# Optimization experiments

Hardware: AMD Instinct MI355X
Metric: run time of the kernel (lower is better)

Reference implementation:

```python
import jax, jax.numpy as jnp
import numpy as np

B, T, C, H = 8, 1024, 1024, 16  # batch, seq, n_embd, n_head


def setup_inputs() -> dict:
    key = jax.random.key(0)
    ks = jax.random.split(key, 5)
    scale = 1.0 / np.sqrt(C)
    return {
        "x": jax.random.normal(ks[0], (B, T, C), dtype=jnp.float32),
        "Wqkv": jax.random.normal(ks[1], (C, 3 * C), dtype=jnp.float32) * scale,
        "bqkv": jax.random.normal(ks[2], (3 * C,), dtype=jnp.float32) * 0.02,
        "Wproj": jax.random.normal(ks[3], (C, C), dtype=jnp.float32) * scale,
        "bproj": jax.random.normal(ks[4], (C,), dtype=jnp.float32) * 0.02,
        "n_head": H,
    }


def reference(x, Wqkv, bqkv, Wproj, bproj, n_head):
    Bb, Tt, Cc = x.shape
    hd = Cc // n_head  # head dim
    qkv = x @ Wqkv + bqkv                      # [B,T,3C]
    q, k, v = jnp.split(qkv, 3, axis=-1)       # each [B,T,C]
    # [B,T,C] -> [B,H,T,hd]
    def to_heads(t):
        return t.reshape(Bb, Tt, n_head, hd).transpose(0, 2, 1, 3)
    q, k, v = to_heads(q), to_heads(k), to_heads(v)
    scores = jnp.einsum("bhqd,bhkd->bhqk", q, k) / jnp.sqrt(jnp.asarray(hd, q.dtype))
    causal = jnp.tril(jnp.ones((Tt, Tt), dtype=bool))
    scores = jnp.where(causal, scores, jnp.asarray(-jnp.inf, scores.dtype))
    attn = jax.nn.softmax(scores, axis=-1)
    y = jnp.einsum("bhqk,bhkd->bhqd", attn, v)  # [B,H,T,hd]
    y = y.transpose(0, 2, 1, 3).reshape(Bb, Tt, Cc)
    return y @ Wproj + bproj
```

## Files before the change

### kernel.cpp

```cpp
#include <hip/hip_runtime.h>
#include <hip/hip_bf16.h>
#include <math.h>
#include <type_traits>

#define Bz 8
#define Tz 1024
#define Cz 1024
#define Hz 16
#define HDz 64
#define Mz (Bz*Tz)
#define N1 (3*Cz)

typedef __attribute__((ext_vector_type(8))) short short8;
typedef __attribute__((ext_vector_type(4))) short short4v;
typedef __attribute__((ext_vector_type(4))) float floatx4;

__device__ __forceinline__ unsigned short f2bf(float f) {
    unsigned u = __float_as_uint(f);
    return (unsigned short)((u + 0x7FFFu + ((u >> 16) & 1u)) >> 16);
}

__device__ __forceinline__ unsigned pkbf(float a, float b) {
    __hip_bfloat162 h = __float22bfloat162_rn(make_float2(a, b));
    return *(unsigned*)&h;
}

__device__ __forceinline__ void gload16(const void* g, void* l) {
    __builtin_amdgcn_global_load_lds(
        (const __attribute__((address_space(1))) unsigned int*)g,
        (__attribute__((address_space(3))) unsigned int*)l, 16, 0, 0);
}

__global__ __launch_bounds__(256) void prep_kernel(
    const float* __restrict__ x, unsigned short* __restrict__ xb,
    const float* __restrict__ Wqkv, unsigned short* __restrict__ Wqkvt,
    const float* __restrict__ Wproj, unsigned short* __restrict__ Wprojt)
{
    __shared__ float tile[32][33];
    const int bid = blockIdx.x;
    const int tid = threadIdx.x;
    if (bid < 8192) {
        int i = bid * 256 + tid;
        float4 v = *(const float4*)&x[(size_t)i * 4];
        ushort4 o;
        o.x = f2bf(v.x); o.y = f2bf(v.y); o.z = f2bf(v.z); o.w = f2bf(v.w);
        *(ushort4*)&xb[(size_t)i * 4] = o;
        return;
    }
    const float* W; unsigned short* Wt; int K, N, n0, k0;
    if (bid < 11264) {
        int b = bid - 8192;  W = Wqkv;  Wt = Wqkvt;  K = Cz; N = N1;
        n0 = (b % 96) * 32;  k0 = (b / 96) * 32;
    } else {
        int b = bid - 11264; W = Wproj; Wt = Wprojt; K = Cz; N = Cz;
        n0 = (b % 32) * 32;  k0 = (b / 32) * 32;
    }
    const int tx = tid & 31, ty = tid >> 5;
#pragma unroll
    for (int i = 0; i < 4; ++i)
        tile[ty + i * 8][tx] = W[(size_t)(k0 + ty + i * 8) * N + n0 + tx];
    __syncthreads();
#pragma unroll
    for (int i = 0; i < 4; ++i)
        Wt[(size_t)(n0 + ty + i * 8) * K + k0 + tx] = f2bf(tile[tx][ty + i * 8]);
}

__global__ __launch_bounds__(256) void vtrans_kernel(const unsigned short* __restrict__ qkvb,
    unsigned short* __restrict__ Vt)
{
    __shared__ unsigned short tile[64][72];
    const int t0 = blockIdx.x * 64;
    const int bh = blockIdx.y;
    const int b = bh >> 4, h = bh & 15;
    const int tid = threadIdx.x;
#pragma unroll
    for (int it = 0; it < 2; ++it) {
        int idx = tid + it * 256;
        int tl = idx >> 3, d8 = idx & 7;
        *(short8*)&tile[tl][d8 * 8] =
            *(const short8*)&qkvb[(size_t)(b * Tz + t0 + tl) * N1 + 2 * Cz + h * HDz + d8 * 8];
    }
    __syncthreads();
#pragma unroll
    for (int it = 0; it < 2; ++it) {
        int idx = tid + it * 256;
        int d = idx >> 3, t8 = idx & 7;
        unsigned short o[8];
#pragma unroll
        for (int j = 0; j < 8; ++j) o[j] = tile[t8 * 8 + j][d];
        *(short8*)&Vt[(size_t)bh * (HDz * Tz) + (size_t)d * Tz + t0 + t8 * 8] = *(short8*)o;
    }
}

__global__ __launch_bounds__(256) void gemm_kernel(const unsigned short* __restrict__ A,
    const unsigned short* __restrict__ Bt, const float* __restrict__ bias,
    void* __restrict__ Cout, int M, int N, int K, int outBf16)
{
    __shared__ unsigned short As[128 * 64];
    __shared__ unsigned short Bs[128 * 64];
    const int tid = threadIdx.x;
    const int lane = tid & 63;
    const int w = tid >> 6, wr = w >> 1, wc = w & 1;
    const int quad = lane >> 4, m16 = lane & 15;
    const int row0 = blockIdx.y * 128, col0 = blockIdx.x * 128;

    float bv[4];
#pragma unroll
    for (int ni = 0; ni < 4; ++ni)
        bv[ni] = bias[col0 + wc * 64 + ni * 16 + m16];

    floatx4 acc[4][4];
#pragma unroll
    for (int mi = 0; mi < 4; ++mi)
#pragma unroll
        for (int ni = 0; ni < 4; ++ni)
            acc[mi][ni] = (floatx4){0.f, 0.f, 0.f, 0.f};

    const int l3 = lane >> 3;
    const int swz = ((lane & 7) ^ l3) * 8;
    const unsigned short* gA[4];
    const unsigned short* gB[4];
    unsigned short* lA[4];
    unsigned short* lB[4];
#pragma unroll
    for (int i = 0; i < 4; ++i) {
        int c = w * 4 + i;
        gA[i] = A  + (size_t)(row0 + c * 8 + l3) * K + swz;
        gB[i] = Bt + (size_t)(col0 + c * 8 + l3) * K + swz;
        lA[i] = &As[c * 512];
        lB[i] = &Bs[c * 512];
    }
    const int sw7 = m16 & 7;

    for (int k0 = 0; k0 < K; k0 += 64) {
#pragma unroll
        for (int i = 0; i < 4; ++i) {
            gload16(gA[i] + k0, lA[i]);
            gload16(gB[i] + k0, lB[i]);
        }
        __syncthreads();
#pragma unroll
        for (int s = 0; s < 2; ++s) {
            short8 af[4], bfr[4];
            const int ch = ((s * 4 + quad) ^ sw7) * 8;
#pragma unroll
            for (int mi = 0; mi < 4; ++mi)
                af[mi] = *(short8*)&As[(wr * 64 + mi * 16 + m16) * 64 + ch];
#pragma unroll
            for (int ni = 0; ni < 4; ++ni)
                bfr[ni] = *(short8*)&Bs[(wc * 64 + ni * 16 + m16) * 64 + ch];
#pragma unroll
            for (int mi = 0; mi < 4; ++mi)
#pragma unroll
                for (int ni = 0; ni < 4; ++ni)
                    acc[mi][ni] = __builtin_amdgcn_mfma_f32_16x16x32_bf16(af[mi], bfr[ni], acc[mi][ni], 0, 0, 0);
        }
        __syncthreads();
    }

#pragma unroll
    for (int mi = 0; mi < 4; ++mi)
#pragma unroll
        for (int ni = 0; ni < 4; ++ni)
#pragma unroll
            for (int reg = 0; reg < 4; ++reg) {
                int r = row0 + wr * 64 + mi * 16 + quad * 4 + reg;
                int c = col0 + wc * 64 + ni * 16 + m16;
                float v = acc[mi][ni][reg] + bv[ni];
                if (outBf16) ((unsigned short*)Cout)[(size_t)r * N + c] = f2bf(v);
                else         ((float*)Cout)[(size_t)r * N + c] = v;
            }
}

__global__ __launch_bounds__(128) void attn_kernel(const unsigned short* __restrict__ qkvb,
    const unsigned short* __restrict__ VtG, unsigned short* __restrict__ attb)
{
    __shared__ unsigned short Ks[2][64 * 64];
    __shared__ unsigned short Vs[2][64 * 64];

    const int bx = blockIdx.x;
    const int bh = blockIdx.y;
    const int b = bh >> 4, h = bh & 15;
    const int tid = threadIdx.x, lane = tid & 63, w = tid >> 6;
    const int quad = lane >> 4, m16 = lane & 15;
    const int qis[2] = {15 - bx, bx};

    const unsigned short* Kb = qkvb + (size_t)(b * Tz) * N1 + Cz + h * HDz;
    const unsigned short* Vb = VtG + (size_t)bh * (HDz * Tz);

    const int l3 = lane >> 3, l7 = lane & 7;
    const int gsw = ((l7 ^ l3) << 3);
    const int sw = m16 & 7;
    const int p0 = (quad ^ sw) << 3;

    short8 onesf = (short8){0,0,0,0,0,0,0,0};
    if (m16 == 0) {
        const short one = (short)0x3F80;
        onesf = (short8){one,one,one,one,one,one,one,one};
    }

    int srow[4];
#pragma unroll
    for (int i = 0; i < 4; ++i) srow[i] = w * 32 + i * 8 + l3;

#pragma unroll
    for (int i = 0; i < 4; ++i) {
        gload16(Kb + (size_t)srow[i] * N1 + gsw, &Ks[0][(w * 4 + i) * 512]);
        gload16(Vb + (size_t)srow[i] * Tz + gsw, &Vs[0][(w * 4 + i) * 512]);
    }

    int buf = 0;
    for (int t = 0; t < 2; ++t) {
        const int qi = qis[t];

        short8 qf[2][2];
        int qrow[2];
#pragma unroll
        for (int mi = 0; mi < 2; ++mi) {
            qrow[mi] = qi * 64 + w * 32 + mi * 16 + m16;
            const size_t rq = (size_t)(b * Tz + qrow[mi]) * N1 + h * HDz;
            qf[mi][0] = *(const short8*)&qkvb[rq + quad * 8];
            qf[mi][1] = *(const short8*)&qkvb[rq + 32 + quad * 8];
        }

        floatx4 of[2][4];
#pragma unroll
        for (int mi = 0; mi < 2; ++mi)
#pragma unroll
            for (int dc = 0; dc < 4; ++dc) of[mi][dc] = (floatx4){0.f, 0.f, 0.f, 0.f};
        floatx4 lsum[2];
        lsum[0] = (floatx4){0.f, 0.f, 0.f, 0.f};
        lsum[1] = (floatx4){0.f, 0.f, 0.f, 0.f};

        auto tile_body = [&](auto diag_c) {
            constexpr bool DIAG = decltype(diag_c)::value;
            constexpr int M0MAX = 4;
            short8 pf[2][2];
#pragma unroll
            for (int m0 = 0; m0 < M0MAX; ++m0) {
                if (DIAG && w == 0 && m0 >= 2) continue;
                const unsigned short* kr = &Ks[buf][(m0 * 16 + m16) * 64];
                short8 kf0 = *(const short8*)&kr[p0];
                short8 kf1 = *(const short8*)&kr[p0 ^ 32];
#pragma unroll
                for (int mi = 0; mi < 2; ++mi) {
                    floatx4 st = (floatx4){0.f, 0.f, 0.f, 0.f};
                    st = __builtin_amdgcn_mfma_f32_16x16x32_bf16(kf0, qf[mi][0], st, 0, 0, 0);
                    st = __builtin_amdgcn_mfma_f32_16x16x32_bf16(kf1, qf[mi][1], st, 0, 0, 0);
                    float p[4];
#pragma unroll
                    for (int reg = 0; reg < 4; ++reg) {
                        p[reg] = exp2f(st[reg] * 0.18033688f);
                        if (DIAG) {
                            int key = m0 * 16 + quad * 4 + reg;
                            int qr  = w * 32 + mi * 16 + m16;
                            p[reg] = (key <= qr) ? p[reg] : 0.f;
                        }
                    }
                    unsigned* pp = (unsigned*)&pf[mi][m0 >> 1];
                    pp[(m0 & 1) * 2 + 0] = pkbf(p[0], p[1]);
                    pp[(m0 & 1) * 2 + 1] = pkbf(p[2], p[3]);
                }
            }
#pragma unroll
            for (int kg = 0; kg < 2; ++kg) {
                if (DIAG && w == 0 && kg == 1) continue;
#pragma unroll
                for (int mi = 0; mi < 2; ++mi)
                    lsum[mi] = __builtin_amdgcn_mfma_f32_16x16x32_bf16(onesf, pf[mi][kg], lsum[mi], 0, 0, 0);
#pragma unroll
                for (int dc = 0; dc < 4; ++dc) {
                    const unsigned short* vrow = &Vs[buf][(dc * 16 + m16) * 64];
                    const int g0 = kg * 4 + (quad >> 1);
                    const int off = (quad & 1) * 4;
                    short4v v0 = *(const short4v*)&vrow[((g0 ^ sw) << 3) + off];
                    short4v v1 = *(const short4v*)&vrow[(((g0 + 2) ^ sw) << 3) + off];
                    short8 vf;
                    vf[0] = v0[0]; vf[1] = v0[1]; vf[2] = v0[2]; vf[3] = v0[3];
                    vf[4] = v1[0]; vf[5] = v1[1]; vf[6] = v1[2]; vf[7] = v1[3];
#pragma unroll
                    for (int mi = 0; mi < 2; ++mi)
                        of[mi][dc] = __builtin_amdgcn_mfma_f32_16x16x32_bf16(vf, pf[mi][kg], of[mi][dc], 0, 0, 0);
                }
            }
        };

        for (int ki = 0; ki <= qi; ++ki) {
            __syncthreads();
            const int nk = (ki < qi) ? (ki + 1) : (t == 0 ? 0 : -1);
            if (nk >= 0) {
                const size_t ko = (size_t)nk * 64;
#pragma unroll
                for (int i = 0; i < 4; ++i) {
                    gload16(Kb + (ko + srow[i]) * N1 + gsw, &Ks[buf ^ 1][(w * 4 + i) * 512]);
                    gload16(Vb + (size_t)srow[i] * Tz + ko + gsw, &Vs[buf ^ 1][(w * 4 + i) * 512]);
                }
            }
            if (ki == qi) tile_body(std::true_type{});
            else          tile_body(std::false_type{});
            buf ^= 1;
        }

#pragma unroll
        for (int mi = 0; mi < 2; ++mi) {
            const float l = __shfl(lsum[mi][0], m16);
            const float inv = 1.f / l;
            const size_t orow = (size_t)(b * Tz + qrow[mi]) * Cz + h * HDz;
#pragma unroll
            for (int dc = 0; dc < 4; ++dc) {
                ushort4 o;
                o.x = f2bf(of[mi][dc][0] * inv);
                o.y = f2bf(of[mi][dc][1] * inv);
                o.z = f2bf(of[mi][dc][2] * inv);
                o.w = f2bf(of[mi][dc][3] * inv);
                *(ushort4*)&attb[orow + dc * 16 + quad * 4] = o;
            }
        }
    }
}

extern "C" void kernel_launch(void* const* d_in, const int* in_sizes, int n_in,
                              void* d_out, int out_size, void* d_ws, size_t ws_size,
                              hipStream_t stream)
{
    const float* x     = (const float*)d_in[0];
    const float* Wqkv  = (const float*)d_in[1];
    const float* bqkv  = (const float*)d_in[2];
    const float* Wproj = (const float*)d_in[3];
    const float* bproj = (const float*)d_in[4];
    float* out = (float*)d_out;

    unsigned short* xb     = (unsigned short*)d_ws;
    unsigned short* Wqkvt  = xb + (size_t)Mz * Cz;
    unsigned short* Wprojt = Wqkvt + (size_t)N1 * Cz;
    unsigned short* qkvb   = Wprojt + (size_t)Cz * Cz;
    unsigned short* VtG    = qkvb + (size_t)Mz * N1;
    unsigned short* attb   = VtG + (size_t)(Bz * Hz) * HDz * Tz;

    prep_kernel<<<12288, 256, 0, stream>>>(x, xb, Wqkv, Wqkvt, Wproj, Wprojt);

    gemm_kernel<<<dim3(N1 / 128, Mz / 128), 256, 0, stream>>>(
        xb, Wqkvt, bqkv, qkvb, Mz, N1, Cz, 1);

    vtrans_kernel<<<dim3(Tz / 64, Bz * Hz), 256, 0, stream>>>(qkvb, VtG);

    attn_kernel<<<dim3(8, Bz * Hz), 128, 0, stream>>>(qkvb, VtG, attb);

    gemm_kernel<<<dim3(Cz / 128, Mz / 128), 256, 0, stream>>>(
        attb, Wprojt, bproj, out, Mz, Cz, Cz, 0);
}
```

Before: 251.0 us.

## Fuse V transpose into QKV GEMM epilogue and drop vtrans kernel

The QKV GEMM epilogue now writes Q and K as bf16 into a narrower 2048-column buffer. For V column tiles it stages the tile transposed in shared memory and writes it straight into the head-major V^T layout used by attention. This removes the separate vtrans launch along with the V write and re-read through global memory. The attention output also reuses the xb workspace region. The cost is a larger shared-memory footprint in the GEMM and an extra sync on the V tiles.

New measurement: 247.6 us. No clear change (-1.4%).

```diff
diff --git a/kernel.cpp b/kernel.cpp
--- a/kernel.cpp
+++ b/kernel.cpp
@@ -10,6 +10,7 @@
 #define HDz 64
 #define Mz (Bz*Tz)
 #define N1 (3*Cz)
+#define QKN 2048
 
 typedef __attribute__((ext_vector_type(8))) short short8;
 typedef __attribute__((ext_vector_type(4))) short short4v;
@@ -65,39 +66,14 @@
         Wt[(size_t)(n0 + ty + i * 8) * K + k0 + tx] = f2bf(tile[tx][ty + i * 8]);
 }
 
-__global__ __launch_bounds__(256) void vtrans_kernel(const unsigned short* __restrict__ qkvb,
-    unsigned short* __restrict__ Vt)
-{
-    __shared__ unsigned short tile[64][72];
-    const int t0 = blockIdx.x * 64;
-    const int bh = blockIdx.y;
-    const int b = bh >> 4, h = bh & 15;
-    const int tid = threadIdx.x;
-#pragma unroll
-    for (int it = 0; it < 2; ++it) {
-        int idx = tid + it * 256;
-        int tl = idx >> 3, d8 = idx & 7;
-        *(short8*)&tile[tl][d8 * 8] =
-            *(const short8*)&qkvb[(size_t)(b * Tz + t0 + tl) * N1 + 2 * Cz + h * HDz + d8 * 8];
-    }
-    __syncthreads();
-#pragma unroll
-    for (int it = 0; it < 2; ++it) {
-        int idx = tid + it * 256;
-        int d = idx >> 3, t8 = idx & 7;
-        unsigned short o[8];
-#pragma unroll
-        for (int j = 0; j < 8; ++j) o[j] = tile[t8 * 8 + j][d];
-        *(short8*)&Vt[(size_t)bh * (HDz * Tz) + (size_t)d * Tz + t0 + t8 * 8] = *(short8*)o;
-    }
-}
-
 __global__ __launch_bounds__(256) void gemm_kernel(const unsigned short* __restrict__ A,
     const unsigned short* __restrict__ Bt, const float* __restrict__ bias,
-    void* __restrict__ Cout, int M, int N, int K, int outBf16)
+    void* __restrict__ Cout, unsigned short* __restrict__ VtG,
+    int M, int N, int K, int mode)
 {
-    __shared__ unsigned short As[128 * 64];
-    __shared__ unsigned short Bs[128 * 64];
+    __shared__ unsigned short smem[17408];
+    unsigned short* As = smem;
+    unsigned short* Bs = smem + 8192;
     const int tid = threadIdx.x;
     const int lane = tid & 63;
     const int w = tid >> 6, wr = w >> 1, wc = w & 1;
@@ -158,21 +134,56 @@
         __syncthreads();
     }
 
-#pragma unroll
-    for (int mi = 0; mi < 4; ++mi)
-#pragma unroll
-        for (int ni = 0; ni < 4; ++ni)
-#pragma unroll
-            for (int reg = 0; reg < 4; ++reg) {
-                int r = row0 + wr * 64 + mi * 16 + quad * 4 + reg;
-                int c = col0 + wc * 64 + ni * 16 + m16;
-                float v = acc[mi][ni][reg] + bv[ni];
-                if (outBf16) ((unsigned short*)Cout)[(size_t)r * N + c] = f2bf(v);
-                else         ((float*)Cout)[(size_t)r * N + c] = v;
-            }
-}
-
-__global__ __launch_bounds__(128) void attn_kernel(const unsigned short* __restrict__ qkvb,
+    if (mode == 0) {
+#pragma unroll
+        for (int mi = 0; mi < 4; ++mi)
+#pragma unroll
+            for (int ni = 0; ni < 4; ++ni)
+#pragma unroll
+                for (int reg = 0; reg < 4; ++reg) {
+                    int r = row0 + wr * 64 + mi * 16 + quad * 4 + reg;
+                    int c = col0 + wc * 64 + ni * 16 + m16;
+                    ((float*)Cout)[(size_t)r * N + c] = acc[mi][ni][reg] + bv[ni];
+                }
+    } else if (col0 < 2048) {
+#pragma unroll
+        for (int mi = 0; mi < 4; ++mi)
+#pragma unroll
+            for (int ni = 0; ni < 4; ++ni)
+#pragma unroll
+                for (int reg = 0; reg < 4; ++reg) {
+                    int r = row0 + wr * 64 + mi * 16 + quad * 4 + reg;
+                    int c = col0 + wc * 64 + ni * 16 + m16;
+                    ((unsigned short*)Cout)[(size_t)r * QKN + c] = f2bf(acc[mi][ni][reg] + bv[ni]);
+                }
+    } else {
+        unsigned short* vt = smem;
+        const int hb = (col0 - 2048) >> 6;
+#pragma unroll
+        for (int mi = 0; mi < 4; ++mi)
+#pragma unroll
+            for (int ni = 0; ni < 4; ++ni) {
+                const int d  = ni * 16 + m16;
+                const int lr = wr * 64 + mi * 16 + quad * 4;
+                unsigned* dst = (unsigned*)&vt[(wc * 64 + d) * 136 + lr];
+                dst[0] = pkbf(acc[mi][ni][0] + bv[ni], acc[mi][ni][1] + bv[ni]);
+                dst[1] = pkbf(acc[mi][ni][2] + bv[ni], acc[mi][ni][3] + bv[ni]);
+            }
+        __syncthreads();
+        const int wsel = tid >> 7;
+        const int d    = (tid >> 1) & 63;
+        const int tseg = (tid & 1) * 64;
+        const unsigned short* src = &vt[(wsel * 64 + d) * 136 + tseg];
+        unsigned short* dstg = VtG
+            + (size_t)((row0 >> 10) * Hz + hb + wsel) * (HDz * Tz)
+            + (size_t)d * Tz + (row0 & 1023) + tseg;
+#pragma unroll
+        for (int k = 0; k < 8; ++k)
+            *(short8*)&dstg[k * 8] = *(const short8*)&src[k * 8];
+    }
+}
+
+__global__ __launch_bounds__(128) void attn_kernel(const unsigned short* __restrict__ qkb,
     const unsigned short* __restrict__ VtG, unsigned short* __restrict__ attb)
 {
     __shared__ unsigned short Ks[2][64 * 64];
@@ -185,7 +196,7 @@
     const int quad = lane >> 4, m16 = lane & 15;
     const int qis[2] = {15 - bx, bx};
 
-    const unsigned short* Kb = qkvb + (size_t)(b * Tz) * N1 + Cz + h * HDz;
+    const unsigned short* Kb = qkb + (size_t)(b * Tz) * QKN + Cz + h * HDz;
     const unsigned short* Vb = VtG + (size_t)bh * (HDz * Tz);
 
     const int l3 = lane >> 3, l7 = lane & 7;
@@ -205,7 +216,7 @@
 
 #pragma unroll
     for (int i = 0; i < 4; ++i) {
-        gload16(Kb + (size_t)srow[i] * N1 + gsw, &Ks[0][(w * 4 + i) * 512]);
+        gload16(Kb + (size_t)srow[i] * QKN + gsw, &Ks[0][(w * 4 + i) * 512]);
         gload16(Vb + (size_t)srow[i] * Tz + gsw, &Vs[0][(w * 4 + i) * 512]);
     }
 
@@ -218,9 +229,9 @@
 #pragma unroll
         for (int mi = 0; mi < 2; ++mi) {
             qrow[mi] = qi * 64 + w * 32 + mi * 16 + m16;
-            const size_t rq = (size_t)(b * Tz + qrow[mi]) * N1 + h * HDz;
-            qf[mi][0] = *(const short8*)&qkvb[rq + quad * 8];
-            qf[mi][1] = *(const short8*)&qkvb[rq + 32 + quad * 8];
+            const size_t rq = (size_t)(b * Tz + qrow[mi]) * QKN + h * HDz;
+            qf[mi][0] = *(const short8*)&qkb[rq + quad * 8];
+            qf[mi][1] = *(const short8*)&qkb[rq + 32 + quad * 8];
         }
 
         floatx4 of[2][4];
@@ -234,10 +245,9 @@
 
         auto tile_body = [&](auto diag_c) {
             constexpr bool DIAG = decltype(diag_c)::value;
-            constexpr int M0MAX = 4;
             short8 pf[2][2];
 #pragma unroll
-            for (int m0 = 0; m0 < M0MAX; ++m0) {
+            for (int m0 = 0; m0 < 4; ++m0) {
                 if (DIAG && w == 0 && m0 >= 2) continue;
                 const unsigned short* kr = &Ks[buf][(m0 * 16 + m16) * 64];
                 short8 kf0 = *(const short8*)&kr[p0];
@@ -292,7 +302,7 @@
                 const size_t ko = (size_t)nk * 64;
 #pragma unroll
                 for (int i = 0; i < 4; ++i) {
-                    gload16(Kb + (ko + srow[i]) * N1 + gsw, &Ks[buf ^ 1][(w * 4 + i) * 512]);
+                    gload16(Kb + (ko + srow[i]) * QKN + gsw, &Ks[buf ^ 1][(w * 4 + i) * 512]);
                     gload16(Vb + (size_t)srow[i] * Tz + ko + gsw, &Vs[buf ^ 1][(w * 4 + i) * 512]);
                 }
             }
@@ -333,19 +343,17 @@
     unsigned short* xb     = (unsigned short*)d_ws;
     unsigned short* Wqkvt  = xb + (size_t)Mz * Cz;
     unsigned short* Wprojt = Wqkvt + (size_t)N1 * Cz;
-    unsigned short* qkvb   = Wprojt + (size_t)Cz * Cz;
-    unsigned short* VtG    = qkvb + (size_t)Mz * N1;
-    unsigned short* attb   = VtG + (size_t)(Bz * Hz) * HDz * Tz;
+    unsigned short* qkb    = Wprojt + (size_t)Cz * Cz;
+    unsigned short* VtG    = qkb + (size_t)Mz * QKN;
+    unsigned short* attb   = xb;
 
     prep_kernel<<<12288, 256, 0, stream>>>(x, xb, Wqkv, Wqkvt, Wproj, Wprojt);
 
     gemm_kernel<<<dim3(N1 / 128, Mz / 128), 256, 0, stream>>>(
-        xb, Wqkvt, bqkv, qkvb, Mz, N1, Cz, 1);
-
-    vtrans_kernel<<<dim3(Tz / 64, Bz * Hz), 256, 0, stream>>>(qkvb, VtG);
-
-    attn_kernel<<<dim3(8, Bz * Hz), 128, 0, stream>>>(qkvb, VtG, attb);
+        xb, Wqkvt, bqkv, qkb, VtG, Mz, N1, Cz, 2);
+
+    attn_kernel<<<dim3(8, Bz * Hz), 128, 0, stream>>>(qkb, VtG, attb);
 
     gemm_kernel<<<dim3(Cz / 128, Mz / 128), 256, 0, stream>>>(
-        attb, Wprojt, bproj, out, Mz, Cz, Cz, 0);
-}
+        attb, Wprojt, bproj, out, nullptr, Mz, Cz, Cz, 0);
+}
```
